# Kernel optimization log

Measured on AMD Instinct MI355X. Metric: run time of the kernel, lower is better.

The kernel has to match this reference:

```python
import jax, jax.numpy as jnp
import numpy as np

N = 100000      # nodes
E = 6400000     # edges
F_IN = 128      # input feature dim (lazily inferred by PyG)
C = 2           # out_channels (hard-coded in module)
NEG_SLOPE = 0.2 # GATConv default leaky_relu slope


def setup_inputs() -> dict:
    key = jax.random.key(0)
    ks = jax.random.split(key, 8)
    x = jax.random.normal(ks[0], (N, F_IN), dtype=jnp.float32)
    edge_index = jax.random.randint(ks[1], (2, E), 0, N, dtype=jnp.int64)
    edge_attr = jax.random.normal(ks[2], (E, 1), dtype=jnp.float32)
    s = 1.0 / np.sqrt(F_IN)
    W_src = (jax.random.normal(ks[3], (F_IN, C), dtype=jnp.float32) * s)
    W_edge = jax.random.normal(ks[4], (1, C), dtype=jnp.float32)
    att_src = jax.random.normal(ks[5], (C,), dtype=jnp.float32)
    att_dst = jax.random.normal(ks[6], (C,), dtype=jnp.float32)
    att_edge = jax.random.normal(ks[7], (C,), dtype=jnp.float32)
    bias = jnp.zeros((C,), dtype=jnp.float32)
    return {"x": x, "edge_index": edge_index, "edge_attr": edge_attr,
            "W_src": W_src, "W_edge": W_edge, "att_src": att_src,
            "att_dst": att_dst, "att_edge": att_edge, "bias": bias}


def reference(x, edge_index, edge_attr, W_src, W_edge, att_src, att_dst, att_edge, bias):
    src, dst = edge_index[0], edge_index[1]
    # Single-tensor input in PyG GATConv -> x_src = x_dst = lin_src(x)
    h = x @ W_src                      # [N, C]  (heads=1 folded away)
    a_src = h @ att_src                # [N]
    a_dst = h @ att_dst                # [N]
    he = edge_attr @ W_edge            # [E, C]
    a_e = he @ att_edge                # [E]
    # per-edge attention logit
    alpha = a_src[src] + a_dst[dst] + a_e
    alpha = jax.nn.leaky_relu(alpha, NEG_SLOPE)
    # segment softmax over incoming edges of each destination node
    amax = jax.ops.segment_max(alpha, dst, num_segments=N)
    amax = jnp.where(jnp.isfinite(amax), amax, 0.0)  # empty segments
    ex = jnp.exp(alpha - amax[dst])
    denom = jax.ops.segment_sum(ex, dst, num_segments=N)
    alpha_n = ex / (denom[dst] + 1e-16)
    # weighted scatter-add aggregation
    msg = h[src] * alpha_n[:, None]    # [E, C]
    out = jax.ops.segment_sum(msg, dst, num_segments=N) + bias  # [N, C]
    return out, alpha_n[:, None]       # alpha: [E, heads=1]
```

## Files before the change

kernel.cpp:

```cpp
#include <hip/hip_runtime.h>
#include <hip/hip_fp16.h>

#define NN 100000
#define NE 6400000
#define NEG_SLOPE 0.2f

#define NBIN 32
#define BSLICE 3125
#define NCH 16
#define ABLK 512
#define EPB (NE / ABLK)
#define RND 4096
#define CAP 256
#define NODEBLK 1024

#define FSLICE 10240
#define FNSLICE 10
#define FNCHUNK 20
#define FCHUNK (NE / FNCHUNK)

__global__ void gat_node_hist(const float* __restrict__ x, const float* __restrict__ W,
                              const float* __restrict__ att_src, const float* __restrict__ att_dst,
                              float4* __restrict__ pack, float* __restrict__ asrc,
                              float* __restrict__ adst,
                              const int* __restrict__ dst, int* __restrict__ cnt) {
    if (blockIdx.x < NODEBLK) {
        int gtid = blockIdx.x * 256 + threadIdx.x;
        int wave = gtid >> 6, lane = threadIdx.x & 63;
        const int nw = (NODEBLK * 256) >> 6;
        float as0 = att_src[0], as1 = att_src[1];
        float ad0 = att_dst[0], ad1 = att_dst[1];
        for (int node = wave; node < NN; node += nw) {
            float2 xx = *(const float2*)(x + (size_t)node * 128 + lane * 2);
            float2 w0 = *(const float2*)(W + lane * 4);
            float2 w1 = *(const float2*)(W + lane * 4 + 2);
            float c0 = xx.x * w0.x + xx.y * w1.x;
            float c1 = xx.x * w0.y + xx.y * w1.y;
            #pragma unroll
            for (int off = 32; off; off >>= 1) {
                c0 += __shfl_down(c0, off);
                c1 += __shfl_down(c1, off);
            }
            if (lane == 0) {
                float s = c0 * as0 + c1 * as1;
                float d = c0 * ad0 + c1 * ad1;
                pack[node] = make_float4(c0, c1, s, d);
                asrc[node] = s;
                adst[node] = d;
            }
        }
    } else {
        __shared__ unsigned h[NBIN];
        const int ablk = blockIdx.x - NODEBLK, t = threadIdx.x;
        if (t < NBIN) h[t] = 0;
        __syncthreads();
        const int b0 = ablk * EPB;
        for (int o = t * 4; o < EPB; o += 1024) {
            int4 d4 = *(const int4*)(dst + b0 + o);
            const int* dp = (const int*)&d4;
            #pragma unroll
            for (int u = 0; u < 4; ++u)
                atomicAdd(&h[(unsigned)dp[u] / BSLICE], 1u);
        }
        __syncthreads();
        if (t < NBIN) cnt[t * ABLK + ablk] = (int)h[t];
    }
}

__global__ __launch_bounds__(1024) void
gat_prefix(int* __restrict__ cnt, int* __restrict__ binstart) {
    __shared__ int btot[NBIN];
    __shared__ int bst[NBIN + 1];
    const int t = threadIdx.x, w = t >> 6, l = t & 63;
    int c[2][8], s[2], incl[2];
    #pragma unroll
    for (int q = 0; q < 2; ++q) {
        const int b = w + q * 16;
        int* row = cnt + b * ABLK;
        int ss = 0;
        #pragma unroll
        for (int j = 0; j < 8; ++j) { c[q][j] = row[l * 8 + j]; ss += c[q][j]; }
        int inc = ss;
        #pragma unroll
        for (int d = 1; d < 64; d <<= 1) {
            int v = __shfl_up(inc, d);
            if (l >= d) inc += v;
        }
        if (l == 63) btot[b] = inc;
        s[q] = ss; incl[q] = inc;
    }
    __syncthreads();
    if (t == 0) {
        int run = 0;
        for (int b = 0; b < NBIN; ++b) { bst[b] = run; run += btot[b]; }
        bst[NBIN] = run;
    }
    __syncthreads();
    #pragma unroll
    for (int q = 0; q < 2; ++q) {
        const int b = w + q * 16;
        int* row = cnt + b * ABLK;
        int base = bst[b] + incl[q] - s[q];
        #pragma unroll
        for (int j = 0; j < 8; ++j) { row[l * 8 + j] = base; base += c[q][j]; }
    }
    if (t <= NBIN) binstart[t] = bst[t];
}

__global__ __launch_bounds__(1024) void
gat_scatter(const int* __restrict__ src, const int* __restrict__ dst,
            const float* __restrict__ ea, const float4* __restrict__ pack,
            const float* __restrict__ adst,
            const float* __restrict__ W_edge, const float* __restrict__ att_edge,
            const int* __restrict__ base, uint2* __restrict__ recs,
            __half* __restrict__ elog) {
    __shared__ uint2 stage[NBIN][CAP];
    __shared__ unsigned cur[NBIN], flushed[NBIN], bbase[NBIN];
    const int ablk = blockIdx.x, t = threadIdx.x;
    if (t < NBIN) {
        cur[t] = 0; flushed[t] = 0;
        bbase[t] = (unsigned)base[t * ABLK + ablk];
    }
    __syncthreads();
    const float k = W_edge[0] * att_edge[0] + W_edge[1] * att_edge[1];
    const int b0 = ablk * EPB;
    const int nrounds = (EPB + RND - 1) / RND;

    for (int r = 0; r < nrounds; ++r) {
        const int lim = EPB - r * RND;
        const bool act = (t * 4) < lim;
        const int o = act ? (r * RND + t * 4) : 0;
        const int i = b0 + o;
        int4 s4 = *(const int4*)(src + i);
        int4 d4 = *(const int4*)(dst + i);
        float4 e4 = *(const float4*)(ea + i);
        const int* sp = (const int*)&s4;
        const int* dp = (const int*)&d4;
        const float* ep = (const float*)&e4;
        float4 ps[4];
        float  ad[4];
        #pragma unroll
        for (int u = 0; u < 4; ++u) {
            ps[u] = pack[sp[u]];
            ad[u] = adst[dp[u]];
        }
        float al[4];
        #pragma unroll
        for (int u = 0; u < 4; ++u) {
            float a = ps[u].z + ad[u] + k * ep[u];
            al[u] = a > 0.0f ? a : NEG_SLOPE * a;
        }
        if (act) {
            if (elog) {
                uint2 ev;
                ev.x = (unsigned)__half_as_ushort(__float2half_rn(al[0])) |
                       ((unsigned)__half_as_ushort(__float2half_rn(al[1])) << 16);
                ev.y = (unsigned)__half_as_ushort(__float2half_rn(al[2])) |
                       ((unsigned)__half_as_ushort(__float2half_rn(al[3])) << 16);
                *(uint2*)(elog + i) = ev;
            }
            #pragma unroll
            for (int u = 0; u < 4; ++u) {
                unsigned d = (unsigned)dp[u];
                unsigned bin = d / BSLICE;
                unsigned off = d - bin * BSLICE;
                unsigned pos = atomicAdd(&cur[bin], 1u);
                unsigned hh = (unsigned)__half_as_ushort(__float2half_rn(ps[u].x)) |
                              ((unsigned)__half_as_ushort(__float2half_rn(ps[u].y)) << 16);
                unsigned lo = (unsigned)__half_as_ushort(__float2half_rn(al[u])) | (off << 16);
                stage[bin][pos & (CAP - 1)] = make_uint2(hh, lo);
            }
        }
        __syncthreads();
        const int w = t >> 6, l = t & 63;
        const bool last = (r == nrounds - 1);
        for (int b = w * 2; b < w * 2 + 2; ++b) {
            unsigned start = flushed[b];
            unsigned n = cur[b] - start;
            if (!last) n &= ~15u;
            if (n) {
                size_t gb = (size_t)bbase[b] + start;
                for (unsigned j = l; j < n; j += 64)
                    recs[gb + j] = stage[b][(start + j) & (CAP - 1)];
                if (l == 0) flushed[b] = start + n;
            }
        }
        __syncthreads();
    }
}

__global__ __launch_bounds__(1024) void
gat_scan(const uint2* __restrict__ recs, const int* __restrict__ binstart,
         float* __restrict__ partial) {
    __shared__ float   dacc[BSLICE];
    __shared__ __half2 hacc[BSLICE];
    const int blk = blockIdx.x, t = threadIdx.x;
    const int b = blk / NCH, c = blk % NCH;
    for (int j = t; j < BSLICE; j += 1024) {
        dacc[j] = 0.f;
        hacc[j] = __floats2half2_rn(0.f, 0.f);
    }
    __syncthreads();
    const int s0 = binstart[b], len = binstart[b + 1] - s0;
    const int c0 = s0 + (int)((long long)len * c / NCH);
    const int c1 = s0 + (int)((long long)len * (c + 1) / NCH);

#define PROC(r)                                                                \
    do {                                                                       \
        unsigned off_ = (r).y >> 16;                                           \
        float al_ = __half2float(__ushort_as_half((unsigned short)((r).y & 0xFFFFu))); \
        float ex_ = __expf(al_);                                               \
        float h0_ = __half2float(__ushort_as_half((unsigned short)((r).x & 0xFFFFu))); \
        float h1_ = __half2float(__ushort_as_half((unsigned short)((r).x >> 16)));     \
        atomicAdd(&dacc[off_], ex_);                                           \
        unsafeAtomicAdd(&hacc[off_], __floats2half2_rn(ex_ * h0_, ex_ * h1_)); \
    } while (0)

    int i = c0 + t;
    for (; i + 3072 < c1; i += 4096) {
        uint2 r0 = recs[i], r1 = recs[i + 1024], r2 = recs[i + 2048], r3 = recs[i + 3072];
        PROC(r0); PROC(r1); PROC(r2); PROC(r3);
    }
    for (; i < c1; i += 1024) {
        uint2 r = recs[i];
        PROC(r);
    }
#undef PROC
    __syncthreads();
    float* p = partial + (size_t)blk * (2 * BSLICE);
    unsigned* pu = (unsigned*)(p + BSLICE);
    const unsigned* hb = (const unsigned*)hacc;
    for (int j = t; j < BSLICE; j += 1024) {
        p[j] = dacc[j];
        pu[j] = hb[j];
    }
}

__global__ void gat_combine(const float* __restrict__ partial,
                            const float* __restrict__ adst,
                            const float* __restrict__ bias,
                            float* __restrict__ out, float2* __restrict__ adiv) {
    int n = blockIdx.x * blockDim.x + threadIdx.x;
    if (n >= NN) return;
    int b = n / BSLICE, off = n % BSLICE;
    const float* pbase = partial + (size_t)(b * NCH) * (2 * BSLICE);
    float de = 0.f, n0 = 0.f, n1 = 0.f;
    for (int c = 0; c < NCH; ++c) {
        const float* p = pbase + (size_t)c * (2 * BSLICE);
        de += p[off];
        unsigned hb = ((const unsigned*)p)[BSLICE + off];
        float2 hf = __half22float2(*(const __half2*)&hb);
        n0 += hf.x; n1 += hf.y;
    }
    float inv = 1.0f / (de + 1e-16f);
    out[2 * n]     = n0 * inv + bias[0];
    out[2 * n + 1] = n1 * inv + bias[1];
    adiv[n] = make_float2(adst[n], inv);
}

__global__ void gat_alpha_fast(const int* __restrict__ dst, const __half* __restrict__ elog,
                               const float2* __restrict__ adiv, float* __restrict__ alpha) {
    int i = (blockIdx.x * blockDim.x + threadIdx.x) * 4;
    if (i >= NE) return;
    int4 d4 = *(const int4*)(dst + i);
    uint2 ev = *(const uint2*)(elog + i);
    const int* dp = (const int*)&d4;
    float iv[4];
    #pragma unroll
    for (int u = 0; u < 4; ++u) iv[u] = adiv[dp[u]].y;
    float al[4] = {
        __half2float(__ushort_as_half((unsigned short)(ev.x & 0xFFFFu))),
        __half2float(__ushort_as_half((unsigned short)(ev.x >> 16))),
        __half2float(__ushort_as_half((unsigned short)(ev.y & 0xFFFFu))),
        __half2float(__ushort_as_half((unsigned short)(ev.y >> 16)))};
    float4 a;
    float* ap = (float*)&a;
    #pragma unroll
    for (int u = 0; u < 4; ++u) ap[u] = __expf(al[u]) * iv[u];
    *(float4*)(alpha + i) = a;
}

__global__ void gat_alpha(const int* __restrict__ src, const int* __restrict__ dst,
                          const float* __restrict__ ea,
                          const float* __restrict__ asrc, const float2* __restrict__ adiv,
                          const float* __restrict__ W_edge, const float* __restrict__ att_edge,
                          float* __restrict__ alpha) {
    const float k = W_edge[0] * att_edge[0] + W_edge[1] * att_edge[1];
    int i = (blockIdx.x * blockDim.x + threadIdx.x) * 4;
    if (i >= NE) return;
    int4   d4 = *(const int4*)(dst + i);
    int4   s4 = *(const int4*)(src + i);
    float4 e4 = *(const float4*)(ea + i);
    const int*   dp = (const int*)&d4;
    const int*   sp = (const int*)&s4;
    const float* ep = (const float*)&e4;
    float  as[4];
    float2 av[4];
    #pragma unroll
    for (int u = 0; u < 4; ++u) {
        as[u] = asrc[sp[u]];
        av[u] = adiv[dp[u]];
    }
    float4 a;
    float* ap = (float*)&a;
    #pragma unroll
    for (int u = 0; u < 4; ++u) {
        float al = as[u] + av[u].x + k * ep[u];
        al = al > 0.0f ? al : NEG_SLOPE * al;
        ap[u] = __expf(al) * av[u].y;
    }
    *(float4*)(alpha + i) = a;
}

__global__ void gat_node_fb(const float* __restrict__ x, const float* __restrict__ W,
                            const float* __restrict__ att_src, const float* __restrict__ att_dst,
                            float4* __restrict__ pack, float* __restrict__ asrc,
                            float* __restrict__ adst, int n) {
    int gtid = blockIdx.x * blockDim.x + threadIdx.x;
    int wave = gtid >> 6, lane = threadIdx.x & 63;
    int nw = (gridDim.x * blockDim.x) >> 6;
    float as0 = att_src[0], as1 = att_src[1];
    float ad0 = att_dst[0], ad1 = att_dst[1];
    for (int node = wave; node < n; node += nw) {
        float2 xx = *(const float2*)(x + (size_t)node * 128 + lane * 2);
        float2 w0 = *(const float2*)(W + lane * 4);
        float2 w1 = *(const float2*)(W + lane * 4 + 2);
        float c0 = xx.x * w0.x + xx.y * w1.x;
        float c1 = xx.x * w0.y + xx.y * w1.y;
        #pragma unroll
        for (int off = 32; off; off >>= 1) {
            c0 += __shfl_down(c0, off);
            c1 += __shfl_down(c1, off);
        }
        if (lane == 0) {
            float s = c0 * as0 + c1 * as1;
            float d = c0 * ad0 + c1 * ad1;
            pack[node] = make_float4(c0, c1, s, d);
            asrc[node] = s;
            adst[node] = d;
        }
    }
}

__global__ __launch_bounds__(1024) void
gat_scan_fb(const int* __restrict__ src, const int* __restrict__ dst,
            const float* __restrict__ ea, const float4* __restrict__ pack,
            const float* __restrict__ adst,
            const float* __restrict__ W_edge, const float* __restrict__ att_edge,
            float* __restrict__ partial) {
    __shared__ float sacc[FSLICE * 3];
    const int s = blockIdx.x / FNCHUNK;
    const int c = blockIdx.x % FNCHUNK;
    const int lo = s * FSLICE;
    for (int j = threadIdx.x; j < FSLICE * 3; j += 1024) sacc[j] = 0.0f;
    __syncthreads();
    const float k = W_edge[0] * att_edge[0] + W_edge[1] * att_edge[1];
    const int base = c * FCHUNK;
    for (int o = threadIdx.x * 8; o < FCHUNK; o += 1024 * 8) {
        const int i = base + o;
        int4   da = *(const int4*)(dst + i), db = *(const int4*)(dst + i + 4);
        int4   sa = *(const int4*)(src + i), sb = *(const int4*)(src + i + 4);
        float4 e0 = *(const float4*)(ea + i), e1 = *(const float4*)(ea + i + 4);
        int   dd[8] = {da.x, da.y, da.z, da.w, db.x, db.y, db.z, db.w};
        int   ss[8] = {sa.x, sa.y, sa.z, sa.w, sb.x, sb.y, sb.z, sb.w};
        float ee[8] = {e0.x, e0.y, e0.z, e0.w, e1.x, e1.y, e1.z, e1.w};
        unsigned off[8];
        float4 ps[8];
        float  ad[8];
        #pragma unroll
        for (int u = 0; u < 8; ++u) {
            off[u] = (unsigned)(dd[u] - lo);
            bool acc = off[u] < FSLICE;
            ps[u] = pack[acc ? ss[u] : 0];
            ad[u] = adst[acc ? dd[u] : lo];
        }
        #pragma unroll
        for (int u = 0; u < 8; ++u) {
            float al = ps[u].z + ad[u] + k * ee[u];
            al = al > 0.0f ? al : NEG_SLOPE * al;
            float ex = __expf(al);
            if (off[u] < FSLICE) {
                atomicAdd(&sacc[off[u] * 3],     ex);
                atomicAdd(&sacc[off[u] * 3 + 1], ex * ps[u].x);
                atomicAdd(&sacc[off[u] * 3 + 2], ex * ps[u].y);
            }
        }
    }
    __syncthreads();
    float* pout = partial + (size_t)blockIdx.x * (FSLICE * 3);
    for (int j = threadIdx.x; j < FSLICE * 3; j += 1024) pout[j] = sacc[j];
}

__global__ void gat_combine_fb(const float* __restrict__ partial,
                               const float* __restrict__ adst,
                               const float* __restrict__ bias,
                               float* __restrict__ out, float2* __restrict__ adiv) {
    int n = blockIdx.x * blockDim.x + threadIdx.x;
    if (n >= NN) return;
    int sl = n / FSLICE, off = n % FSLICE;
    const float* p = partial + (size_t)sl * FNCHUNK * (FSLICE * 3) + (size_t)off * 3;
    float de = 0.f, n0 = 0.f, n1 = 0.f;
    for (int c = 0; c < FNCHUNK; ++c, p += FSLICE * 3) {
        de += p[0]; n0 += p[1]; n1 += p[2];
    }
    float inv = 1.0f / (de + 1e-16f);
    out[2 * n]     = n0 * inv + bias[0];
    out[2 * n + 1] = n1 * inv + bias[1];
    adiv[n] = make_float2(adst[n], inv);
}

extern "C" void kernel_launch(void* const* d_in, const int* in_sizes, int n_in,
                              void* d_out, int out_size, void* d_ws, size_t ws_size,
                              hipStream_t stream) {
    const float* x        = (const float*)d_in[0];
    const int*   ei       = (const int*)  d_in[1];
    const float* ea       = (const float*)d_in[2];
    const float* W_src    = (const float*)d_in[3];
    const float* W_edge   = (const float*)d_in[4];
    const float* att_src  = (const float*)d_in[5];
    const float* att_dst  = (const float*)d_in[6];
    const float* att_edge = (const float*)d_in[7];
    const float* bias     = (const float*)d_in[8];

    float* out   = (float*)d_out;
    float* alpha = out + 2 * NN;

    const int* src = ei;
    const int* dst = ei + NE;

    size_t fixed = (size_t)NE * 8 + (size_t)NN * 16 + 2 * (size_t)NN * 4
                 + (size_t)NN * 8 + (size_t)NBIN * ABLK * 4
                 + (NBIN + 1) * 4 + 256;
    size_t need_mid  = fixed;
    size_t need_fast = fixed + (size_t)NE * 2;

    if (ws_size >= need_mid) {
        uint2*    recs = (uint2*)d_ws;
        float4*   pack = (float4*)((char*)d_ws + (size_t)NE * 8);
        float*    asrc = (float*)(pack + NN);
        float*    adst = asrc + NN;
        float2*   adiv = (float2*)(adst + NN);
        int*      cnt  = (int*)(adiv + NN);
        int*      binstart = cnt + NBIN * ABLK;
        __half*   elog = (ws_size >= need_fast) ? (__half*)(binstart + NBIN + 1 + 32) : nullptr;
        float*    partial = alpha;

        gat_node_hist<<<NODEBLK + ABLK, 256, 0, stream>>>(x, W_src, att_src, att_dst,
                                                          pack, asrc, adst, dst, cnt);
        gat_prefix  <<<1, 1024, 0, stream>>>(cnt, binstart);
        gat_scatter <<<ABLK, 1024, 0, stream>>>(src, dst, ea, pack, adst,
                                                W_edge, att_edge, cnt, recs, elog);
        gat_scan    <<<NBIN * NCH, 1024, 0, stream>>>(recs, binstart, partial);
        gat_combine <<<(NN + 255) / 256, 256, 0, stream>>>(partial, adst, bias, out, adiv);
        if (elog)
            gat_alpha_fast<<<NE / (256 * 4), 256, 0, stream>>>(dst, elog, adiv, alpha);
        else
            gat_alpha<<<NE / (256 * 4), 256, 0, stream>>>(src, dst, ea, asrc, adiv,
                                                          W_edge, att_edge, alpha);
    } else {
        float4* pack = (float4*)d_ws;
        float*  asrc = (float*)(pack + NN);
        float*  adst = asrc + NN;
        float2* adiv = (float2*)(adst + NN);
        float*  partial = alpha;

        gat_node_fb   <<<1024, 256, 0, stream>>>(x, W_src, att_src, att_dst, pack, asrc, adst, NN);
        gat_scan_fb   <<<FNSLICE * FNCHUNK, 1024, 0, stream>>>(src, dst, ea, pack, adst,
                                                               W_edge, att_edge, partial);
        gat_combine_fb<<<(NN + 255) / 256, 256, 0, stream>>>(partial, adst, bias, out, adiv);
        gat_alpha     <<<NE / (256 * 4), 256, 0, stream>>>(src, dst, ea, asrc, adiv,
                                                           W_edge, att_edge, alpha);
    }
}
```

Before: 198.1 us.

## Shrink node pack to 8 bytes, pad LDS staging rows, deepen scan unroll

Node features are packed as two fp16 values plus the fp32 source logit in 8 bytes instead of a 16-byte float4. This halves the random-gather traffic in the scatter kernel and removes the per-edge fp16 conversion there. LDS staging rows are padded to 257 entries to reduce bank conflicts. The scan loop now issues 8 loads per iteration instead of 4, and the adiv float2 array is replaced by a separate inverse-denominator array so the alpha kernels gather only 4 bytes per edge. The extra unrolling may raise register pressure in the scan kernel.

```diff
diff --git a/kernel.cpp b/kernel.cpp
--- a/kernel.cpp
+++ b/kernel.cpp
@@ -12,6 +12,7 @@
 #define EPB (NE / ABLK)
 #define RND 4096
 #define CAP 256
+#define SROW 257
 #define NODEBLK 1024
 
 #define FSLICE 10240
@@ -21,7 +22,7 @@
 
 __global__ void gat_node_hist(const float* __restrict__ x, const float* __restrict__ W,
                               const float* __restrict__ att_src, const float* __restrict__ att_dst,
-                              float4* __restrict__ pack, float* __restrict__ asrc,
+                              uint2* __restrict__ pack8, float* __restrict__ asrc,
                               float* __restrict__ adst,
                               const int* __restrict__ dst, int* __restrict__ cnt) {
     if (blockIdx.x < NODEBLK) {
@@ -44,7 +45,9 @@
             if (lane == 0) {
                 float s = c0 * as0 + c1 * as1;
                 float d = c0 * ad0 + c1 * ad1;
-                pack[node] = make_float4(c0, c1, s, d);
+                unsigned h01 = (unsigned)__half_as_ushort(__float2half_rn(c0)) |
+                               ((unsigned)__half_as_ushort(__float2half_rn(c1)) << 16);
+                pack8[node] = make_uint2(h01, __float_as_uint(s));
                 asrc[node] = s;
                 adst[node] = d;
             }
@@ -109,12 +112,12 @@
 
 __global__ __launch_bounds__(1024) void
 gat_scatter(const int* __restrict__ src, const int* __restrict__ dst,
-            const float* __restrict__ ea, const float4* __restrict__ pack,
+            const float* __restrict__ ea, const uint2* __restrict__ pack8,
             const float* __restrict__ adst,
             const float* __restrict__ W_edge, const float* __restrict__ att_edge,
             const int* __restrict__ base, uint2* __restrict__ recs,
             __half* __restrict__ elog) {
-    __shared__ uint2 stage[NBIN][CAP];
+    __shared__ uint2 stage[NBIN * SROW];
     __shared__ unsigned cur[NBIN], flushed[NBIN], bbase[NBIN];
     const int ablk = blockIdx.x, t = threadIdx.x;
     if (t < NBIN) {
@@ -137,17 +140,17 @@
         const int* sp = (const int*)&s4;
         const int* dp = (const int*)&d4;
         const float* ep = (const float*)&e4;
-        float4 ps[4];
-        float  ad[4];
+        uint2 ps[4];
+        float ad[4];
         #pragma unroll
         for (int u = 0; u < 4; ++u) {
-            ps[u] = pack[sp[u]];
+            ps[u] = pack8[sp[u]];
             ad[u] = adst[dp[u]];
         }
         float al[4];
         #pragma unroll
         for (int u = 0; u < 4; ++u) {
-            float a = ps[u].z + ad[u] + k * ep[u];
+            float a = __uint_as_float(ps[u].y) + ad[u] + k * ep[u];
             al[u] = a > 0.0f ? a : NEG_SLOPE * a;
         }
         if (act) {
@@ -165,10 +168,8 @@
                 unsigned bin = d / BSLICE;
                 unsigned off = d - bin * BSLICE;
                 unsigned pos = atomicAdd(&cur[bin], 1u);
-                unsigned hh = (unsigned)__half_as_ushort(__float2half_rn(ps[u].x)) |
-                              ((unsigned)__half_as_ushort(__float2half_rn(ps[u].y)) << 16);
                 unsigned lo = (unsigned)__half_as_ushort(__float2half_rn(al[u])) | (off << 16);
-                stage[bin][pos & (CAP - 1)] = make_uint2(hh, lo);
+                stage[bin * SROW + (pos & (CAP - 1))] = make_uint2(ps[u].x, lo);
             }
         }
         __syncthreads();
@@ -181,7 +182,7 @@
             if (n) {
                 size_t gb = (size_t)bbase[b] + start;
                 for (unsigned j = l; j < n; j += 64)
-                    recs[gb + j] = stage[b][(start + j) & (CAP - 1)];
+                    recs[gb + j] = stage[b * SROW + ((start + j) & (CAP - 1))];
                 if (l == 0) flushed[b] = start + n;
             }
         }
@@ -217,9 +218,13 @@
     } while (0)
 
     int i = c0 + t;
-    for (; i + 3072 < c1; i += 4096) {
-        uint2 r0 = recs[i], r1 = recs[i + 1024], r2 = recs[i + 2048], r3 = recs[i + 3072];
+    for (; i + 7 * 1024 < c1; i += 8 * 1024) {
+        uint2 r0 = recs[i],          r1 = recs[i + 1024];
+        uint2 r2 = recs[i + 2048],   r3 = recs[i + 3072];
+        uint2 r4 = recs[i + 4096],   r5 = recs[i + 5120];
+        uint2 r6 = recs[i + 6144],   r7 = recs[i + 7168];
         PROC(r0); PROC(r1); PROC(r2); PROC(r3);
+        PROC(r4); PROC(r5); PROC(r6); PROC(r7);
     }
     for (; i < c1; i += 1024) {
         uint2 r = recs[i];
@@ -237,9 +242,8 @@
 }
 
 __global__ void gat_combine(const float* __restrict__ partial,
-                            const float* __restrict__ adst,
                             const float* __restrict__ bias,
-                            float* __restrict__ out, float2* __restrict__ adiv) {
+                            float* __restrict__ out, float* __restrict__ invd) {
     int n = blockIdx.x * blockDim.x + threadIdx.x;
     if (n >= NN) return;
     int b = n / BSLICE, off = n % BSLICE;
@@ -255,11 +259,11 @@
     float inv = 1.0f / (de + 1e-16f);
     out[2 * n]     = n0 * inv + bias[0];
     out[2 * n + 1] = n1 * inv + bias[1];
-    adiv[n] = make_float2(adst[n], inv);
+    invd[n] = inv;
 }
 
 __global__ void gat_alpha_fast(const int* __restrict__ dst, const __half* __restrict__ elog,
-                               const float2* __restrict__ adiv, float* __restrict__ alpha) {
+                               const float* __restrict__ invd, float* __restrict__ alpha) {
     int i = (blockIdx.x * blockDim.x + threadIdx.x) * 4;
     if (i >= NE) return;
     int4 d4 = *(const int4*)(dst + i);
@@ -267,7 +271,7 @@
     const int* dp = (const int*)&d4;
     float iv[4];
     #pragma unroll
-    for (int u = 0; u < 4; ++u) iv[u] = adiv[dp[u]].y;
+    for (int u = 0; u < 4; ++u) iv[u] = invd[dp[u]];
     float al[4] = {
         __half2float(__ushort_as_half((unsigned short)(ev.x & 0xFFFFu))),
         __half2float(__ushort_as_half((unsigned short)(ev.x >> 16))),
@@ -282,7 +286,8 @@
 
 __global__ void gat_alpha(const int* __restrict__ src, const int* __restrict__ dst,
                           const float* __restrict__ ea,
-                          const float* __restrict__ asrc, const float2* __restrict__ adiv,
+                          const float* __restrict__ asrc, const float* __restrict__ adst,
+                          const float* __restrict__ invd,
                           const float* __restrict__ W_edge, const float* __restrict__ att_edge,
                           float* __restrict__ alpha) {
     const float k = W_edge[0] * att_edge[0] + W_edge[1] * att_edge[1];
@@ -294,20 +299,20 @@
     const int*   dp = (const int*)&d4;
     const int*   sp = (const int*)&s4;
     const float* ep = (const float*)&e4;
-    float  as[4];
-    float2 av[4];
+    float as[4], ad[4], iv[4];
     #pragma unroll
     for (int u = 0; u < 4; ++u) {
         as[u] = asrc[sp[u]];
-        av[u] = adiv[dp[u]];
+        ad[u] = adst[dp[u]];
+        iv[u] = invd[dp[u]];
     }
     float4 a;
     float* ap = (float*)&a;
     #pragma unroll
     for (int u = 0; u < 4; ++u) {
-        float al = as[u] + av[u].x + k * ep[u];
+        float al = as[u] + ad[u] + k * ep[u];
         al = al > 0.0f ? al : NEG_SLOPE * al;
-        ap[u] = __expf(al) * av[u].y;
+        ap[u] = __expf(al) * iv[u];
     }
     *(float4*)(alpha + i) = a;
 }
@@ -392,9 +397,8 @@
 }
 
 __global__ void gat_combine_fb(const float* __restrict__ partial,
-                               const float* __restrict__ adst,
                                const float* __restrict__ bias,
-                               float* __restrict__ out, float2* __restrict__ adiv) {
+                               float* __restrict__ out, float* __restrict__ invd) {
     int n = blockIdx.x * blockDim.x + threadIdx.x;
     if (n >= NN) return;
     int sl = n / FSLICE, off = n % FSLICE;
@@ -406,7 +410,7 @@
     float inv = 1.0f / (de + 1e-16f);
     out[2 * n]     = n0 * inv + bias[0];
     out[2 * n + 1] = n1 * inv + bias[1];
-    adiv[n] = make_float2(adst[n], inv);
+    invd[n] = inv;
 }
 
 extern "C" void kernel_launch(void* const* d_in, const int* in_sizes, int n_in,
@@ -428,47 +432,50 @@
     const int* src = ei;
     const int* dst = ei + NE;
 
-    size_t fixed = (size_t)NE * 8 + (size_t)NN * 16 + 2 * (size_t)NN * 4
-                 + (size_t)NN * 8 + (size_t)NBIN * ABLK * 4
-                 + (NBIN + 1) * 4 + 256;
+    size_t fixed = (size_t)NE * 8 + (size_t)NN * 8 + 3 * (size_t)NN * 4
+                 + (size_t)NBIN * ABLK * 4 + (NBIN + 1) * 4 + 512;
     size_t need_mid  = fixed;
     size_t need_fast = fixed + (size_t)NE * 2;
 
     if (ws_size >= need_mid) {
-        uint2*    recs = (uint2*)d_ws;
-        float4*   pack = (float4*)((char*)d_ws + (size_t)NE * 8);
-        float*    asrc = (float*)(pack + NN);
-        float*    adst = asrc + NN;
-        float2*   adiv = (float2*)(adst + NN);
-        int*      cnt  = (int*)(adiv + NN);
-        int*      binstart = cnt + NBIN * ABLK;
-        __half*   elog = (ws_size >= need_fast) ? (__half*)(binstart + NBIN + 1 + 32) : nullptr;
-        float*    partial = alpha;
+        uint2*  recs = (uint2*)d_ws;
+        uint2*  pack8 = (uint2*)((char*)d_ws + (size_t)NE * 8);
+        float*  asrc = (float*)(pack8 + NN);
+        float*  adst = asrc + NN;
+        float*  invd = adst + NN;
+        int*    cnt  = (int*)(invd + NN);
+        int*    binstart = cnt + NBIN * ABLK;
+        __half* elog = nullptr;
+        if (ws_size >= need_fast) {
+            uintptr_t p = ((uintptr_t)(binstart + NBIN + 1) + 255) & ~(uintptr_t)255;
+            elog = (__half*)p;
+        }
+        float*  partial = alpha;
 
         gat_node_hist<<<NODEBLK + ABLK, 256, 0, stream>>>(x, W_src, att_src, att_dst,
-                                                          pack, asrc, adst, dst, cnt);
+                                                          pack8, asrc, adst, dst, cnt);
         gat_prefix  <<<1, 1024, 0, stream>>>(cnt, binstart);
-        gat_scatter <<<ABLK, 1024, 0, stream>>>(src, dst, ea, pack, adst,
+        gat_scatter <<<ABLK, 1024, 0, stream>>>(src, dst, ea, pack8, adst,
                                                 W_edge, att_edge, cnt, recs, elog);
         gat_scan    <<<NBIN * NCH, 1024, 0, stream>>>(recs, binstart, partial);
-        gat_combine <<<(NN + 255) / 256, 256, 0, stream>>>(partial, adst, bias, out, adiv);
+        gat_combine <<<(NN + 255) / 256, 256, 0, stream>>>(partial, bias, out, invd);
         if (elog)
-            gat_alpha_fast<<<NE / (256 * 4), 256, 0, stream>>>(dst, elog, adiv, alpha);
+            gat_alpha_fast<<<NE / (256 * 4), 256, 0, stream>>>(dst, elog, invd, alpha);
         else
-            gat_alpha<<<NE / (256 * 4), 256, 0, stream>>>(src, dst, ea, asrc, adiv,
+            gat_alpha<<<NE / (256 * 4), 256, 0, stream>>>(src, dst, ea, asrc, adst, invd,
                                                           W_edge, att_edge, alpha);
     } else {
         float4* pack = (float4*)d_ws;
         float*  asrc = (float*)(pack + NN);
         float*  adst = asrc + NN;
-        float2* adiv = (float2*)(adst + NN);
+        float*  invd = adst + NN;
         float*  partial = alpha;
 
         gat_node_fb   <<<1024, 256, 0, stream>>>(x, W_src, att_src, att_dst, pack, asrc, adst, NN);
         gat_scan_fb   <<<FNSLICE * FNCHUNK, 1024, 0, stream>>>(src, dst, ea, pack, adst,
                                                                W_edge, att_edge, partial);
-        gat_combine_fb<<<(NN + 255) / 256, 256, 0, stream>>>(partial, adst, bias, out, adiv);
-        gat_alpha     <<<NE / (256 * 4), 256, 0, stream>>>(src, dst, ea, asrc, adiv,
+        gat_combine_fb<<<(NN + 255) / 256, 256, 0, stream>>>(partial, bias, out, invd);
+        gat_alpha     <<<NE / (256 * 4), 256, 0, stream>>>(src, dst, ea, asrc, adst, invd,
                                                            W_edge, att_edge, alpha);
     }
 }
```

Measured after the change: 194.6 us. No clear change (-1.8%).
